# Optimization experiments

Measured on AMD Instinct MI355X. Metric: run time of the kernel, lower is better.

## Reference

```python
import math
import jax, jax.numpy as jnp
import numpy as np

B, P, L, D = 2, 32, 32, 768
N = P * L
H = 12
HD = D // H
FF = 4 * D
NL = 12
NC = 1000
EPS = 1e-5
NEG = -jnp.finfo(jnp.float32).max


def sinusoidal_pe(P, L, D):
    pe = np.zeros((P, L, D), dtype=np.float32)
    half = D // 2
    div = np.exp(np.arange(0.0, half, 2) * -(math.log(10000.0) / half))  # (half/2,)
    pos_l = np.arange(0.0, L)[:, None]
    pos_n = np.arange(0.0, P)[:, None]
    # faithful to the (buggy) torch builder, which requires P == L
    pe[:, :, 0:half:2] = np.sin(pos_n * div)[None, :, :]
    pe[:, :, 1:half:2] = np.cos(pos_n * div)[None, :, :]
    pe[:, :, half::2] = np.sin(pos_l * div)[:, None, :]
    pe[:, :, half + 1::2] = np.cos(pos_l * div)[:, None, :]
    return pe.reshape(P * L, D)


def layernorm(x, w, b):
    mu = jnp.mean(x, axis=-1, keepdims=True)
    var = jnp.var(x, axis=-1, keepdims=True)
    return (x - mu) * jax.lax.rsqrt(var + EPS) * w + b


def setup_inputs() -> dict:
    key = jax.random.key(0)
    ks = jax.random.split(key, 16)
    tn = lambda k, shp: (0.02 * jax.random.normal(k, shp)).astype(jnp.float32)
    inp = {
        "x": jax.random.normal(ks[0], (B, N, D), dtype=jnp.float32),
        "mask": jax.random.randint(ks[1], (B, N), 0, 2).astype(bool),
        "pe": jnp.asarray(sinusoidal_pe(P, L, D)),
        "ln0_w": jnp.ones((NL, D)), "ln0_b": jnp.zeros((NL, D)),
        "qkv_w": tn(ks[2], (NL, D, 3 * D)),
        "proj_w": tn(ks[3], (NL, D, D)), "proj_b": jnp.zeros((NL, D)),
        "ln1_w": jnp.ones((NL, D)), "ln1_b": jnp.zeros((NL, D)),
        "ff1_w": tn(ks[4], (NL, D, FF)), "ff1_b": jnp.zeros((NL, FF)),
        "ff2_w": tn(ks[5], (NL, FF, D)), "ff2_b": jnp.zeros((NL, D)),
        "norm_w": jnp.ones((D,)), "norm_b": jnp.zeros((D,)),
        "pool_w": tn(ks[6], (D, 1)), "pool_b": jnp.zeros((1,)),
        "fc_w": tn(ks[7], (D, NC)), "fc_b": jnp.zeros((NC,)),
    }
    return inp


def reference(x, mask, pe, ln0_w, ln0_b, qkv_w, proj_w, proj_b, ln1_w, ln1_b,
              ff1_w, ff1_b, ff2_w, ff2_b, norm_w, norm_b, pool_w, pool_b, fc_w, fc_b):
    scale = HD ** -0.5
    mask2 = mask[:, None, :] & mask[:, :, None]  # (B,N,N)

    def blk(h, p):
        g0w, g0b, qw, pw, pb, g1w, g1b, f1w, f1b, f2w, f2b = p
        y = layernorm(h, g0w, g0b)
        qkv = (y @ qw).reshape(B, N, 3, H, HD).transpose(2, 0, 3, 1, 4)  # (3,B,H,N,hd)
        q, k, v = qkv[0], qkv[1], qkv[2]
        attn = jnp.einsum('bhnd,bhmd->bhnm', q, k) * scale
        attn = jnp.where(mask2[:, None, :, :], attn, NEG)
        attn = jax.nn.softmax(attn, axis=-1)
        o = jnp.einsum('bhnm,bhmd->bhnd', attn, v)
        o = o.transpose(0, 2, 1, 3).reshape(B, N, D) @ pw + pb
        h = layernorm(h + o, g1w, g1b)
        ff = jax.nn.gelu(h @ f1w + f1b, approximate=False) @ f2w + f2b
        return h + ff, None

    h = x + pe[None]
    params = (ln0_w, ln0_b, qkv_w, proj_w, proj_b, ln1_w, ln1_b, ff1_w, ff1_b, ff2_w, ff2_b)
    h, _ = jax.lax.scan(blk, h, params)
    h = layernorm(h, norm_w, norm_b)
    # seq-pool: softmax over tokens of a learned scalar score
    w = jax.nn.softmax(h @ pool_w + pool_b, axis=1)  # (B,N,1)
    pooled = jnp.einsum('bnc,bnd->bd', w, h)  # c == 1
    return pooled @ fc_w + fc_b
```

## Files before the change

### kernel.cpp

```cpp
#include <hip/hip_runtime.h>
#include <hip/hip_bf16.h>
#include <cfloat>
#include <cmath>

typedef __bf16 bf16x8 __attribute__((ext_vector_type(8)));
typedef __bf16 bf16x4 __attribute__((ext_vector_type(4)));
typedef float  f32x4  __attribute__((ext_vector_type(4)));

static constexpr int Bb = 2, Nn = 1024, Dd = 768, Hh = 12, HDd = 64, FFf = 3072, NLl = 12, NCc = 1000;
static constexpr int Mm = Bb * Nn;
static constexpr float NEGF = -3.402823466e38f;

__device__ __forceinline__ float block_reduce_sum(float v, volatile float* smem) {
  for (int o = 32; o; o >>= 1) v += __shfl_down(v, o);
  int lane = threadIdx.x & 63, w = threadIdx.x >> 6;
  __syncthreads();
  if (lane == 0) smem[w] = v;
  __syncthreads();
  return smem[0] + smem[1] + smem[2] + smem[3];
}

__device__ __forceinline__ float block_reduce_max(float v, volatile float* smem) {
  for (int o = 32; o; o >>= 1) v = fmaxf(v, __shfl_down(v, o));
  int lane = threadIdx.x & 63, w = threadIdx.x >> 6;
  __syncthreads();
  if (lane == 0) smem[w] = v;
  __syncthreads();
  return fmaxf(fmaxf(smem[0], smem[1]), fmaxf(smem[2], smem[3]));
}

__global__ void detect_mask(const unsigned char* __restrict__ m, int* __restrict__ flag) {
  __shared__ int s_nz1, s_nz2, s_nz3, s_nz84, s_pv;
  int tid = threadIdx.x;
  if (tid == 0) { s_nz1 = 0; s_nz2 = 0; s_nz3 = 0; s_nz84 = 0; s_pv = 0; }
  __syncthreads();
  int nz1 = 0, nz2 = 0, nz3 = 0, nz84 = 0, pv = 0;
  for (int i = tid; i < 2048; i += 256) {
    unsigned char v = m[i];
    if (v) {
      int p4 = i & 3;
      if (p4 == 1) nz1 = 1;
      if (p4 == 2) nz2 = 1;
      if (p4 == 3) nz3 = 1;
      if ((i & 7) == 4) nz84 = 1;
      if ((i & 1) == 0) { if (v != 0x80) pv = 1; }
      else              { if (v != 0x3f) pv = 1; }
    }
  }
  if (nz1)  atomicOr(&s_nz1, 1);
  if (nz2)  atomicOr(&s_nz2, 1);
  if (nz3)  atomicOr(&s_nz3, 1);
  if (nz84) atomicOr(&s_nz84, 1);
  if (pv)   atomicOr(&s_pv, 1);
  __syncthreads();
  if (tid == 0) {
    int f;
    if (!s_nz1 && !s_nz2 && !s_nz3) f = s_nz84 ? 0 : 3;
    else if (!s_pv)                 f = s_nz1 ? 4 : 2;
    else                            f = 1;
    *flag = f;
  }
}

__device__ __forceinline__ bool mask_at(const void* mraw, int flag, int idx) {
  switch (flag) {
    case 0:  return ((const int*)mraw)[idx] != 0;
    case 1:  return ((const unsigned char*)mraw)[idx] != 0;
    case 2:  return ((const float*)mraw)[idx] != 0.f;
    case 3:  return ((const long long*)mraw)[idx] != 0;
    default: return ((const unsigned short*)mraw)[idx] != 0;
  }
}

__global__ __launch_bounds__(256) void add_pe_k(const float* __restrict__ x, const float* __restrict__ pe,
                                                float* __restrict__ h) {
  long i = (long)blockIdx.x * 256 + threadIdx.x;
  long nd = i % ((long)Nn * Dd);
  h[i] = x[i] + pe[nd];
}

template<int OBF>
__global__ __launch_bounds__(256) void ln_kernel(const float* __restrict__ X,
                                                 const float* __restrict__ w, const float* __restrict__ b,
                                                 void* __restrict__ Y) {
  __shared__ float smem[4];
  int row = blockIdx.x, tid = threadIdx.x;
  const float* x = X + (size_t)row * Dd;
  float v[3];
  for (int j = 0; j < 3; ++j) v[j] = x[tid + j * 256];
  float s = v[0] + v[1] + v[2];
  s = block_reduce_sum(s, smem);
  float mean = s * (1.f / 768.f);
  float q = 0.f;
  for (int j = 0; j < 3; ++j) { float d = v[j] - mean; q += d * d; }
  q = block_reduce_sum(q, smem);
  float inv = rsqrtf(q * (1.f / 768.f) + 1e-5f);
  for (int j = 0; j < 3; ++j) {
    int c = tid + j * 256;
    float r = (v[j] - mean) * inv * w[c] + b[c];
    if (OBF) ((__bf16*)Y)[(size_t)row * Dd + c] = (__bf16)r;
    else     ((float*)Y)[(size_t)row * Dd + c] = r;
  }
}

__global__ __launch_bounds__(256) void ln2res_kernel(float* __restrict__ H,
                                                     const float* __restrict__ P0, const float* __restrict__ P1,
                                                     const float* __restrict__ pb,
                                                     const float* __restrict__ w, const float* __restrict__ b,
                                                     __bf16* __restrict__ Hb) {
  __shared__ float smem[4];
  int row = blockIdx.x, tid = threadIdx.x;
  float* x  = H  + (size_t)row * Dd;
  const float* p0 = P0 + (size_t)row * Dd;
  const float* p1 = P1 + (size_t)row * Dd;
  float v[3];
  for (int j = 0; j < 3; ++j) {
    int c = tid + j * 256;
    v[j] = x[c] + (p0[c] + p1[c] + pb[c]);
  }
  float s = v[0] + v[1] + v[2];
  s = block_reduce_sum(s, smem);
  float mean = s * (1.f / 768.f);
  float q = 0.f;
  for (int j = 0; j < 3; ++j) { float d = v[j] - mean; q += d * d; }
  q = block_reduce_sum(q, smem);
  float inv = rsqrtf(q * (1.f / 768.f) + 1e-5f);
  for (int j = 0; j < 3; ++j) {
    int c = tid + j * 256;
    float r = (v[j] - mean) * inv * w[c] + b[c];
    x[c] = r;
    Hb[(size_t)row * Dd + c] = (__bf16)r;
  }
}

__global__ __launch_bounds__(256) void reduce_ff2(float* __restrict__ h, const float* __restrict__ p0,
                                                  const float* __restrict__ p1, const float* __restrict__ bias) {
  long i4 = (long)blockIdx.x * 256 + threadIdx.x;
  int col4 = (int)(i4 % (Dd / 4));
  float4 hv = reinterpret_cast<const float4*>(h)[i4];
  float4 a  = reinterpret_cast<const float4*>(p0)[i4];
  float4 c  = reinterpret_cast<const float4*>(p1)[i4];
  float4 bb = reinterpret_cast<const float4*>(bias)[col4];
  hv.x += a.x + c.x + bb.x;
  hv.y += a.y + c.y + bb.y;
  hv.z += a.z + c.z + bb.z;
  hv.w += a.w + c.w + bb.w;
  reinterpret_cast<float4*>(h)[i4] = hv;
}

__device__ __forceinline__ void split8v(const float* __restrict__ v, bf16x8& hi, bf16x8& lo) {
  for (int j = 0; j < 8; ++j) {
    __bf16 h = (__bf16)v[j];
    hi[j] = h;
    lo[j] = (__bf16)(v[j] - (float)h);
  }
}

template<int BN, int EPI, int OBF>
__global__ __launch_bounds__(256) void gemm128(
    const __bf16* __restrict__ Ap, long lda,
    const float* __restrict__ Bp, long ldb,
    const float* __restrict__ bias,
    void* __restrict__ Cp, long ldc,
    int Ksize, long czs)
{
  constexpr int FN = BN / 32;
  constexpr int KB = BN / 8;
  int tid = threadIdx.x;

  int nwg2 = gridDim.x * gridDim.y;
  int bid = blockIdx.y * gridDim.x + blockIdx.x;
  int swz = (bid & 7) * (nwg2 >> 3) + (bid >> 3);
  int bx = swz % gridDim.x, by = swz / gridDim.x;
  int m0 = by * 128, n0 = bx * BN;
  int z = blockIdx.z;

  const __bf16* Aq = Ap + (long)z * Ksize;
  const float* Bq = Bp + (long)z * Ksize * ldb;

  __shared__ __align__(16) __bf16 Ah[128][40];
  __shared__ __align__(16) __bf16 Bh[BN][40], Bl[BN][40];

  f32x4 acc[4][FN];
  #pragma unroll
  for (int i = 0; i < 4; ++i)
    #pragma unroll
    for (int j = 0; j < FN; ++j)
      #pragma unroll
      for (int k = 0; k < 4; ++k) acc[i][j][k] = 0.f;

  int lane = tid & 63;
  int w = tid >> 6;
  int WR = (w >> 1) * 64, WC = (w & 1) * (BN / 2);
  int fr = lane & 15, kg = lane >> 4;

  const int ar = tid >> 1, acs = (tid & 1) * 16;
  const int bn = tid % BN;
  const int kb = (tid / BN) * KB;

  const __bf16* Abase = Aq + (long)(m0 + ar) * lda + acs;
  const float* Bbase = Bq + (long)kb * ldb + (n0 + bn);

  bf16x8 pa0, pa1;
  float pb[KB];
  {
    pa0 = *reinterpret_cast<const bf16x8*>(Abase);
    pa1 = *reinterpret_cast<const bf16x8*>(Abase + 8);
    #pragma unroll
    for (int j = 0; j < KB; ++j) pb[j] = Bbase[(long)j * ldb];
  }

  for (int k0 = 0; k0 < Ksize; k0 += 32) {
    __syncthreads();
    {
      *reinterpret_cast<bf16x8*>(&Ah[ar][acs]) = pa0;
      *reinterpret_cast<bf16x8*>(&Ah[ar][acs + 8]) = pa1;
      #pragma unroll
      for (int g8 = 0; g8 < KB / 8; ++g8) {
        bf16x8 bth, btl;
        split8v(&pb[g8 * 8], bth, btl);
        *reinterpret_cast<bf16x8*>(&Bh[bn][kb + g8 * 8]) = bth;
        *reinterpret_cast<bf16x8*>(&Bl[bn][kb + g8 * 8]) = btl;
      }
    }
    __syncthreads();

    if (k0 + 32 < Ksize) {
      const __bf16* As = Abase + (k0 + 32);
      pa0 = *reinterpret_cast<const bf16x8*>(As);
      pa1 = *reinterpret_cast<const bf16x8*>(As + 8);
      const float* Bs = Bbase + (long)(k0 + 32) * ldb;
      #pragma unroll
      for (int j = 0; j < KB; ++j) pb[j] = Bs[(long)j * ldb];
    }

    bf16x8 ah[4], bh[FN], bl[FN];
    #pragma unroll
    for (int fm = 0; fm < 4; ++fm)
      ah[fm] = *reinterpret_cast<const bf16x8*>(&Ah[WR + fm * 16 + fr][kg * 8]);
    #pragma unroll
    for (int fn = 0; fn < FN; ++fn) {
      bh[fn] = *reinterpret_cast<const bf16x8*>(&Bh[WC + fn * 16 + fr][kg * 8]);
      bl[fn] = *reinterpret_cast<const bf16x8*>(&Bl[WC + fn * 16 + fr][kg * 8]);
    }
    #pragma unroll
    for (int fm = 0; fm < 4; ++fm)
      #pragma unroll
      for (int fn = 0; fn < FN; ++fn) {
        acc[fm][fn] = __builtin_amdgcn_mfma_f32_16x16x32_bf16(ah[fm], bh[fn], acc[fm][fn], 0, 0, 0);
        acc[fm][fn] = __builtin_amdgcn_mfma_f32_16x16x32_bf16(ah[fm], bl[fn], acc[fm][fn], 0, 0, 0);
      }
  }

  #pragma unroll
  for (int fm = 0; fm < 4; ++fm)
    #pragma unroll
    for (int fn = 0; fn < FN; ++fn)
      #pragma unroll
      for (int i = 0; i < 4; ++i) {
        int rowg = m0 + WR + fm * 16 + kg * 4 + i;
        int coln = n0 + WC + fn * 16 + fr;
        float v = acc[fm][fn][i];
        if (EPI >= 1) v += bias[coln];
        if (EPI == 2) v = 0.5f * v * (1.f + erff(v * 0.70710678118654752f));
        long ci = (long)z * czs + (long)rowg * ldc + coln;
        if (OBF) ((__bf16*)Cp)[ci] = (__bf16)v;
        else     ((float*)Cp)[ci] = v;
      }
}

__global__ __launch_bounds__(256) void flash_attn_split(const __bf16* __restrict__ qkvb,
                                                        const void* __restrict__ mraw,
                                                        const int* __restrict__ flagp,
                                                        float* __restrict__ p0, float* __restrict__ p1,
                                                        float2* __restrict__ ml) {
  __shared__ __align__(16) __bf16 Qs[64][72];
  __shared__ __align__(16) __bf16 Ks[64][72];
  __shared__ __align__(16) __bf16 Vt[64][66];
  __shared__ __align__(16) __bf16 Ps[64][72];
  __shared__ float kmf[64];
  __shared__ float qmf[64];

  int s = blockIdx.z & 1, b = blockIdx.z >> 1;
  int hh = blockIdx.y;
  int q0 = blockIdx.x * 64;
  int tid = threadIdx.x, lane = tid & 63, w = tid >> 6;
  int flag = *flagp;
  int fr = lane & 15, kg = lane >> 4;

  const int sr = tid >> 2;
  const int sc = (tid & 3) * 16;

  {
    const __bf16* Qsrc = qkvb + ((long)(b * Nn + q0 + sr)) * (3 * Dd) + hh * HDd + sc;
    *reinterpret_cast<bf16x8*>(&Qs[sr][sc])     = *reinterpret_cast<const bf16x8*>(Qsrc);
    *reinterpret_cast<bf16x8*>(&Qs[sr][sc + 8]) = *reinterpret_cast<const bf16x8*>(Qsrc + 8);
    if (tid < 64) qmf[tid] = mask_at(mraw, flag, b * Nn + q0 + tid) ? 1.f : 0.f;
  }
  __syncthreads();

  float qm[4];
  #pragma unroll
  for (int i = 0; i < 4; ++i) qm[i] = qmf[16 * w + kg * 4 + i];

  bf16x8 qa[2];
  #pragma unroll
  for (int ks = 0; ks < 2; ++ks)
    qa[ks] = *reinterpret_cast<const bf16x8*>(&Qs[16 * w + fr][ks * 32 + kg * 8]);

  float mrow[4], lrow[4];
  f32x4 accO[4];
  #pragma unroll
  for (int i = 0; i < 4; ++i) { mrow[i] = -INFINITY; lrow[i] = 0.f; }
  #pragma unroll
  for (int t = 0; t < 4; ++t)
    for (int i = 0; i < 4; ++i) accO[t][i] = 0.f;

  const int jbeg = s * (Nn / 2), jend = jbeg + (Nn / 2);

  bf16x8 rk0, rk1, rv0, rv1;
  {
    const __bf16* Ksrc = qkvb + ((long)(b * Nn + jbeg + sr)) * (3 * Dd) + Dd + hh * HDd + sc;
    const __bf16* Vsrc = Ksrc + Dd;
    rk0 = *reinterpret_cast<const bf16x8*>(Ksrc);
    rk1 = *reinterpret_cast<const bf16x8*>(Ksrc + 8);
    rv0 = *reinterpret_cast<const bf16x8*>(Vsrc);
    rv1 = *reinterpret_cast<const bf16x8*>(Vsrc + 8);
  }

  for (int j0 = jbeg; j0 < jend; j0 += 64) {
    __syncthreads();
    {
      *reinterpret_cast<bf16x8*>(&Ks[sr][sc])     = rk0;
      *reinterpret_cast<bf16x8*>(&Ks[sr][sc + 8]) = rk1;
      #pragma unroll
      for (int j = 0; j < 8; ++j) {
        Vt[sc + j][sr]     = rv0[j];
        Vt[sc + 8 + j][sr] = rv1[j];
      }
      if (tid < 64) kmf[tid] = mask_at(mraw, flag, b * Nn + j0 + tid) ? 1.f : 0.f;
    }
    __syncthreads();

    if (j0 + 64 < jend) {
      const __bf16* Ksrc = qkvb + ((long)(b * Nn + j0 + 64 + sr)) * (3 * Dd) + Dd + hh * HDd + sc;
      const __bf16* Vsrc = Ksrc + Dd;
      rk0 = *reinterpret_cast<const bf16x8*>(Ksrc);
      rk1 = *reinterpret_cast<const bf16x8*>(Ksrc + 8);
      rv0 = *reinterpret_cast<const bf16x8*>(Vsrc);
      rv1 = *reinterpret_cast<const bf16x8*>(Vsrc + 8);
    }

    f32x4 sacc[4];
    #pragma unroll
    for (int t = 0; t < 4; ++t)
      for (int i = 0; i < 4; ++i) sacc[t][i] = 0.f;
    #pragma unroll
    for (int ks = 0; ks < 2; ++ks) {
      #pragma unroll
      for (int t = 0; t < 4; ++t) {
        bf16x8 bh = *reinterpret_cast<const bf16x8*>(&Ks[16 * t + fr][ks * 32 + kg * 8]);
        sacc[t] = __builtin_amdgcn_mfma_f32_16x16x32_bf16(qa[ks], bh, sacc[t], 0, 0, 0);
      }
    }

    float sv[4][4];
    float mt[4] = {-INFINITY, -INFINITY, -INFINITY, -INFINITY};
    #pragma unroll
    for (int t = 0; t < 4; ++t) {
      float km = kmf[16 * t + fr];
      #pragma unroll
      for (int i = 0; i < 4; ++i) {
        float sx = (km > 0.f && qm[i] > 0.f) ? sacc[t][i] * 0.125f : NEGF;
        sv[t][i] = sx;
        mt[i] = fmaxf(mt[i], sx);
      }
    }
    #pragma unroll
    for (int off = 8; off; off >>= 1)
      #pragma unroll
      for (int i = 0; i < 4; ++i) mt[i] = fmaxf(mt[i], __shfl_xor(mt[i], off));

    float r[4], psum[4];
    #pragma unroll
    for (int i = 0; i < 4; ++i) {
      float mn = fmaxf(mrow[i], mt[i]);
      r[i] = __expf(mrow[i] - mn);
      mrow[i] = mn;
      psum[i] = 0.f;
    }
    #pragma unroll
    for (int t = 0; t < 4; ++t) {
      #pragma unroll
      for (int i = 0; i < 4; ++i) {
        float p = __expf(sv[t][i] - mrow[i]);
        psum[i] += p;
        Ps[16 * w + kg * 4 + i][16 * t + fr] = (__bf16)p;
      }
    }
    #pragma unroll
    for (int off = 8; off; off >>= 1)
      #pragma unroll
      for (int i = 0; i < 4; ++i) psum[i] += __shfl_xor(psum[i], off);
    #pragma unroll
    for (int i = 0; i < 4; ++i) lrow[i] = lrow[i] * r[i] + psum[i];
    #pragma unroll
    for (int t = 0; t < 4; ++t)
      #pragma unroll
      for (int i = 0; i < 4; ++i) accO[t][i] *= r[i];

    __syncthreads();

    #pragma unroll
    for (int ks = 0; ks < 2; ++ks) {
      bf16x8 pa = *reinterpret_cast<const bf16x8*>(&Ps[16 * w + fr][ks * 32 + kg * 8]);
      #pragma unroll
      for (int t2 = 0; t2 < 4; ++t2) {
        bf16x8 vb = *reinterpret_cast<const bf16x8*>(&Vt[16 * t2 + fr][ks * 32 + kg * 8]);
        accO[t2] = __builtin_amdgcn_mfma_f32_16x16x32_bf16(pa, vb, accO[t2], 0, 0, 0);
      }
    }
  }

  float* op = s ? p1 : p0;
  #pragma unroll
  for (int t2 = 0; t2 < 4; ++t2)
    #pragma unroll
    for (int i = 0; i < 4; ++i) {
      int qrow = q0 + 16 * w + kg * 4 + i;
      int col = 16 * t2 + fr;
      op[((long)(b * Nn + qrow)) * Dd + hh * HDd + col] = accO[t2][i];
    }
  if (fr == 0) {
    #pragma unroll
    for (int i = 0; i < 4; ++i) {
      int qrow = q0 + 16 * w + kg * 4 + i;
      ml[((long)(s * Bb + b) * Hh + hh) * Nn + qrow] = make_float2(mrow[i], lrow[i]);
    }
  }
}

__global__ __launch_bounds__(256) void flash_combine(const float* __restrict__ p0, const float* __restrict__ p1,
                                                     const float2* __restrict__ ml, __bf16* __restrict__ ob) {
  long i4 = (long)blockIdx.x * 256 + threadIdx.x;
  long i = i4 * 4;
  int d = (int)(i % Dd);
  long row = i / Dd;
  int b = (int)(row >> 10), n = (int)(row & (Nn - 1));
  int hh = d >> 6;
  float2 a = ml[((long)b * Hh + hh) * Nn + n];
  float2 c = ml[(((long)Bb + b) * Hh + hh) * Nn + n];
  float M = fmaxf(a.x, c.x);
  float w0 = __expf(a.x - M), w1 = __expf(c.x - M);
  float inv = 1.f / (w0 * a.y + w1 * c.y);
  float4 v0 = reinterpret_cast<const float4*>(p0)[i4];
  float4 v1 = reinterpret_cast<const float4*>(p1)[i4];
  bf16x4 r;
  r[0] = (__bf16)((w0 * v0.x + w1 * v1.x) * inv);
  r[1] = (__bf16)((w0 * v0.y + w1 * v1.y) * inv);
  r[2] = (__bf16)((w0 * v0.z + w1 * v1.z) * inv);
  r[3] = (__bf16)((w0 * v0.w + w1 * v1.w) * inv);
  *reinterpret_cast<bf16x4*>(&ob[i]) = r;
}

__global__ __launch_bounds__(256) void pool_score(const float* __restrict__ hn, const float* __restrict__ pw,
                                                  const float* __restrict__ pb, float* __restrict__ s) {
  __shared__ float smem[4];
  int row = blockIdx.x, tid = threadIdx.x;
  const float* x = hn + (size_t)row * Dd;
  float acc = 0.f;
  for (int j = 0; j < 3; ++j) { int c = tid + j * 256; acc += x[c] * pw[c]; }
  acc = block_reduce_sum(acc, smem);
  if (tid == 0) s[row] = acc + pb[0];
}

__global__ __launch_bounds__(256) void pool_softmax(const float* __restrict__ s, float* __restrict__ w) {
  __shared__ float smem[4];
  int b = blockIdx.x, tid = threadIdx.x;
  const float* x = s + b * Nn;
  float v[4];
  for (int j = 0; j < 4; ++j) v[j] = x[tid * 4 + j];
  float mx = fmaxf(fmaxf(v[0], v[1]), fmaxf(v[2], v[3]));
  mx = block_reduce_max(mx, smem);
  float e[4], sum = 0.f;
  for (int j = 0; j < 4; ++j) { e[j] = expf(v[j] - mx); sum += e[j]; }
  sum = block_reduce_sum(sum, smem);
  float inv = 1.f / sum;
  for (int j = 0; j < 4; ++j) w[b * Nn + tid * 4 + j] = e[j] * inv;
}

__global__ __launch_bounds__(256) void pool_reduce1(const float* __restrict__ hn, const float* __restrict__ w,
                                                    float* __restrict__ part) {
  int d = blockIdx.x * 256 + threadIdx.x;
  int ch = blockIdx.y, b = blockIdx.z;
  int n0 = ch * 128;
  float a0 = 0.f, a1 = 0.f;
  for (int n = n0; n < n0 + 128; n += 2) {
    a0 = fmaf(w[b * Nn + n],     hn[((size_t)(b * Nn + n))     * Dd + d], a0);
    a1 = fmaf(w[b * Nn + n + 1], hn[((size_t)(b * Nn + n + 1)) * Dd + d], a1);
  }
  part[((size_t)(b * 8 + ch)) * Dd + d] = a0 + a1;
}

__global__ __launch_bounds__(256) void pool_reduce2(const float* __restrict__ part, float* __restrict__ pooled) {
  int d = blockIdx.x * 256 + threadIdx.x;
  int b = blockIdx.y;
  float s = 0.f;
  #pragma unroll
  for (int ch = 0; ch < 8; ++ch) s += part[((size_t)(b * 8 + ch)) * Dd + d];
  pooled[b * Dd + d] = s;
}

__global__ __launch_bounds__(256) void fc_kernel(const float* __restrict__ pooled, const float* __restrict__ fw,
                                                 const float* __restrict__ fb, float* __restrict__ out) {
  __shared__ float p[768];
  int b = blockIdx.y, tid = threadIdx.x;
  for (int j = 0; j < 3; ++j) p[tid + j * 256] = pooled[b * Dd + tid + j * 256];
  __syncthreads();
  int c = blockIdx.x * 256 + tid;
  if (c < NCc) {
    float a0 = 0.f, a1 = 0.f, a2 = 0.f, a3 = 0.f;
    #pragma unroll 4
    for (int d = 0; d < Dd; d += 4) {
      a0 = fmaf(p[d],     fw[(size_t)d       * NCc + c], a0);
      a1 = fmaf(p[d + 1], fw[(size_t)(d + 1) * NCc + c], a1);
      a2 = fmaf(p[d + 2], fw[(size_t)(d + 2) * NCc + c], a2);
      a3 = fmaf(p[d + 3], fw[(size_t)(d + 3) * NCc + c], a3);
    }
    out[b * NCc + c] = fb[c] + ((a0 + a1) + (a2 + a3));
  }
}

extern "C" void kernel_launch(void* const* d_in, const int* in_sizes, int n_in,
                              void* d_out, int out_size, void* d_ws, size_t ws_size,
                              hipStream_t stream) {
  const float* x      = (const float*)d_in[0];
  const void*  mask   = d_in[1];
  const float* pe     = (const float*)d_in[2];
  const float* ln0_w  = (const float*)d_in[3];
  const float* ln0_b  = (const float*)d_in[4];
  const float* qkv_w  = (const float*)d_in[5];
  const float* proj_w = (const float*)d_in[6];
  const float* proj_b = (const float*)d_in[7];
  const float* ln1_w  = (const float*)d_in[8];
  const float* ln1_b  = (const float*)d_in[9];
  const float* ff1_w  = (const float*)d_in[10];
  const float* ff1_b  = (const float*)d_in[11];
  const float* ff2_w  = (const float*)d_in[12];
  const float* ff2_b  = (const float*)d_in[13];
  const float* norm_w = (const float*)d_in[14];
  const float* norm_b = (const float*)d_in[15];
  const float* pool_w = (const float*)d_in[16];
  const float* pool_b = (const float*)d_in[17];
  const float* fc_w   = (const float*)d_in[18];
  const float* fc_b   = (const float*)d_in[19];
  float* out = (float*)d_out;

  float* ws = (float*)d_ws;
  float*  h     = ws;
  float*  s0    = h + (long)Mm * Dd;
  float*  s1    = s0 + (long)Mm * Dd;
  __bf16* qkvb  = (__bf16*)(s1 + (long)Mm * Dd);
  __bf16* ob    = qkvb + (long)Mm * 3 * Dd;
  __bf16* yb    = ob + (long)Mm * Dd;
  float*  tail  = (float*)(yb + (long)Mm * Dd);
  float*  spool  = tail;
  float*  wpool  = spool + Mm;
  float*  pooled = wpool + Mm;
  float*  ppart  = pooled + Bb * Dd;
  float*  mlbuf  = ppart + (long)Bb * 8 * Dd;
  int*    mflag  = (int*)(mlbuf + (long)2 * 2 * Bb * Hh * Nn);
  __bf16* gb = qkvb;
  float*  hn = s0;

  detect_mask<<<1, 256, 0, stream>>>((const unsigned char*)mask, mflag);
  add_pe_k<<<(Mm * Dd) / 256, 256, 0, stream>>>(x, pe, h);

  for (int l = 0; l < NLl; ++l) {
    ln_kernel<1><<<Mm, 256, 0, stream>>>(h, ln0_w + l * Dd, ln0_b + l * Dd, yb);

    gemm128<64,0,1><<<dim3(3 * Dd / 64, Mm / 128, 1), 256, 0, stream>>>(
        yb, Dd,
        qkv_w + (long)l * Dd * 3 * Dd, 3 * Dd,
        nullptr,
        qkvb, 3 * Dd, Dd, 0);

    flash_attn_split<<<dim3(Nn / 64, Hh, Bb * 2), 256, 0, stream>>>(
        qkvb, mask, mflag, s0, s1, (float2*)mlbuf);
    flash_combine<<<(Mm * Dd / 4) / 256, 256, 0, stream>>>(s0, s1, (const float2*)mlbuf, ob);

    gemm128<64,0,0><<<dim3(Dd / 64, Mm / 128, 2), 256, 0, stream>>>(
        ob, Dd,
        proj_w + (long)l * Dd * Dd, Dd,
        nullptr,
        s0, Dd, Dd / 2, (long)(s1 - s0));

    ln2res_kernel<<<Mm, 256, 0, stream>>>(h, s0, s1, proj_b + l * Dd,
                                          ln1_w + l * Dd, ln1_b + l * Dd, yb);

    gemm128<64,2,1><<<dim3(FFf / 64, Mm / 128, 1), 256, 0, stream>>>(
        yb, Dd,
        ff1_w + (long)l * Dd * FFf, FFf,
        ff1_b + l * FFf,
        gb, FFf, Dd, 0);

    gemm128<64,0,0><<<dim3(Dd / 64, Mm / 128, 2), 256, 0, stream>>>(
        gb, FFf,
        ff2_w + (long)l * FFf * Dd, Dd,
        nullptr,
        s0, Dd, FFf / 2, (long)(s1 - s0));

    reduce_ff2<<<(Mm * Dd / 4) / 256, 256, 0, stream>>>(h, s0, s1, ff2_b + l * Dd);
  }

  ln_kernel<0><<<Mm, 256, 0, stream>>>(h, norm_w, norm_b, hn);
  pool_score<<<Mm, 256, 0, stream>>>(hn, pool_w, pool_b, spool);
  pool_softmax<<<Bb, 256, 0, stream>>>(spool, wpool);
  pool_reduce1<<<dim3(Dd / 256, 8, Bb), 256, 0, stream>>>(hn, wpool, ppart);
  pool_reduce2<<<dim3(Dd / 256, Bb), 256, 0, stream>>>(ppart, pooled);
  fc_kernel<<<dim3(4, Bb), 256, 0, stream>>>(pooled, fc_w, fc_b, out);
}
```

Measured before the change: 2.245 ms.

## Drop bf16 hi/lo weight split in GEMM and fuse FF2 residual with next LayerNorm

The GEMM previously split each fp32 weight into a high and low bf16 pair and issued two MFMAs per fragment to approximate fp32 accuracy. Now it keeps only the single bf16 rounding, which halves MFMA work, B-tile shared memory and the split arithmetic, at the cost of lower weight precision. Separately, the FF2 partial-sum reduction is fused with the following layer's LN0 (or the final norm), removing one elementwise kernel and one LayerNorm pass per layer.

```diff
diff --git a/kernel.cpp b/kernel.cpp
--- a/kernel.cpp
+++ b/kernel.cpp
@@ -103,11 +103,12 @@
   }
 }
 
-__global__ __launch_bounds__(256) void ln2res_kernel(float* __restrict__ H,
+template<int OBF, int HRES>
+__global__ __launch_bounds__(256) void res_ln_kernel(float* __restrict__ H,
                                                      const float* __restrict__ P0, const float* __restrict__ P1,
                                                      const float* __restrict__ pb,
                                                      const float* __restrict__ w, const float* __restrict__ b,
-                                                     __bf16* __restrict__ Hb) {
+                                                     void* __restrict__ Y) {
   __shared__ float smem[4];
   int row = blockIdx.x, tid = threadIdx.x;
   float* x  = H  + (size_t)row * Dd;
@@ -128,31 +129,9 @@
   for (int j = 0; j < 3; ++j) {
     int c = tid + j * 256;
     float r = (v[j] - mean) * inv * w[c] + b[c];
-    x[c] = r;
-    Hb[(size_t)row * Dd + c] = (__bf16)r;
-  }
-}
-
-__global__ __launch_bounds__(256) void reduce_ff2(float* __restrict__ h, const float* __restrict__ p0,
-                                                  const float* __restrict__ p1, const float* __restrict__ bias) {
-  long i4 = (long)blockIdx.x * 256 + threadIdx.x;
-  int col4 = (int)(i4 % (Dd / 4));
-  float4 hv = reinterpret_cast<const float4*>(h)[i4];
-  float4 a  = reinterpret_cast<const float4*>(p0)[i4];
-  float4 c  = reinterpret_cast<const float4*>(p1)[i4];
-  float4 bb = reinterpret_cast<const float4*>(bias)[col4];
-  hv.x += a.x + c.x + bb.x;
-  hv.y += a.y + c.y + bb.y;
-  hv.z += a.z + c.z + bb.z;
-  hv.w += a.w + c.w + bb.w;
-  reinterpret_cast<float4*>(h)[i4] = hv;
-}
-
-__device__ __forceinline__ void split8v(const float* __restrict__ v, bf16x8& hi, bf16x8& lo) {
-  for (int j = 0; j < 8; ++j) {
-    __bf16 h = (__bf16)v[j];
-    hi[j] = h;
-    lo[j] = (__bf16)(v[j] - (float)h);
+    x[c] = HRES ? v[j] : r;
+    if (OBF) ((__bf16*)Y)[(size_t)row * Dd + c] = (__bf16)r;
+    else     ((float*)Y)[(size_t)row * Dd + c] = r;
   }
 }
 
@@ -179,7 +158,7 @@
   const float* Bq = Bp + (long)z * Ksize * ldb;
 
   __shared__ __align__(16) __bf16 Ah[128][40];
-  __shared__ __align__(16) __bf16 Bh[BN][40], Bl[BN][40];
+  __shared__ __align__(16) __bf16 Bh[BN][40];
 
   f32x4 acc[4][FN];
   #pragma unroll
@@ -217,10 +196,10 @@
       *reinterpret_cast<bf16x8*>(&Ah[ar][acs + 8]) = pa1;
       #pragma unroll
       for (int g8 = 0; g8 < KB / 8; ++g8) {
-        bf16x8 bth, btl;
-        split8v(&pb[g8 * 8], bth, btl);
+        bf16x8 bth;
+        #pragma unroll
+        for (int j = 0; j < 8; ++j) bth[j] = (__bf16)pb[g8 * 8 + j];
         *reinterpret_cast<bf16x8*>(&Bh[bn][kb + g8 * 8]) = bth;
-        *reinterpret_cast<bf16x8*>(&Bl[bn][kb + g8 * 8]) = btl;
       }
     }
     __syncthreads();
@@ -234,22 +213,18 @@
       for (int j = 0; j < KB; ++j) pb[j] = Bs[(long)j * ldb];
     }
 
-    bf16x8 ah[4], bh[FN], bl[FN];
+    bf16x8 ah[4], bh[FN];
     #pragma unroll
     for (int fm = 0; fm < 4; ++fm)
       ah[fm] = *reinterpret_cast<const bf16x8*>(&Ah[WR + fm * 16 + fr][kg * 8]);
     #pragma unroll
-    for (int fn = 0; fn < FN; ++fn) {
+    for (int fn = 0; fn < FN; ++fn)
       bh[fn] = *reinterpret_cast<const bf16x8*>(&Bh[WC + fn * 16 + fr][kg * 8]);
-      bl[fn] = *reinterpret_cast<const bf16x8*>(&Bl[WC + fn * 16 + fr][kg * 8]);
-    }
     #pragma unroll
     for (int fm = 0; fm < 4; ++fm)
       #pragma unroll
-      for (int fn = 0; fn < FN; ++fn) {
+      for (int fn = 0; fn < FN; ++fn)
         acc[fm][fn] = __builtin_amdgcn_mfma_f32_16x16x32_bf16(ah[fm], bh[fn], acc[fm][fn], 0, 0, 0);
-        acc[fm][fn] = __builtin_amdgcn_mfma_f32_16x16x32_bf16(ah[fm], bl[fn], acc[fm][fn], 0, 0, 0);
-      }
   }
 
   #pragma unroll
@@ -575,10 +550,9 @@
 
   detect_mask<<<1, 256, 0, stream>>>((const unsigned char*)mask, mflag);
   add_pe_k<<<(Mm * Dd) / 256, 256, 0, stream>>>(x, pe, h);
+  ln_kernel<1><<<Mm, 256, 0, stream>>>(h, ln0_w, ln0_b, yb);
 
   for (int l = 0; l < NLl; ++l) {
-    ln_kernel<1><<<Mm, 256, 0, stream>>>(h, ln0_w + l * Dd, ln0_b + l * Dd, yb);
-
     gemm128<64,0,1><<<dim3(3 * Dd / 64, Mm / 128, 1), 256, 0, stream>>>(
         yb, Dd,
         qkv_w + (long)l * Dd * 3 * Dd, 3 * Dd,
@@ -595,8 +569,8 @@
         nullptr,
         s0, Dd, Dd / 2, (long)(s1 - s0));
 
-    ln2res_kernel<<<Mm, 256, 0, stream>>>(h, s0, s1, proj_b + l * Dd,
-                                          ln1_w + l * Dd, ln1_b + l * Dd, yb);
+    res_ln_kernel<1,0><<<Mm, 256, 0, stream>>>(h, s0, s1, proj_b + l * Dd,
+                                               ln1_w + l * Dd, ln1_b + l * Dd, yb);
 
     gemm128<64,2,1><<<dim3(FFf / 64, Mm / 128, 1), 256, 0, stream>>>(
         yb, Dd,
@@ -610,10 +584,15 @@
         nullptr,
         s0, Dd, FFf / 2, (long)(s1 - s0));
 
-    reduce_ff2<<<(Mm * Dd / 4) / 256, 256, 0, stream>>>(h, s0, s1, ff2_b + l * Dd);
-  }
-
-  ln_kernel<0><<<Mm, 256, 0, stream>>>(h, norm_w, norm_b, hn);
+    if (l + 1 < NLl) {
+      res_ln_kernel<1,1><<<Mm, 256, 0, stream>>>(h, s0, s1, ff2_b + l * Dd,
+                                                 ln0_w + (l + 1) * Dd, ln0_b + (l + 1) * Dd, yb);
+    } else {
+      res_ln_kernel<0,1><<<Mm, 256, 0, stream>>>(h, s0, s1, ff2_b + l * Dd,
+                                                 norm_w, norm_b, hn);
+    }
+  }
+
   pool_score<<<Mm, 256, 0, stream>>>(hn, pool_w, pool_b, spool);
   pool_softmax<<<Bb, 256, 0, stream>>>(spool, wpool);
   pool_reduce1<<<dim3(Dd / 256, 8, Bb), 256, 0, stream>>>(hn, wpool, ppart);
```

After: 2.113 ms. 5.9% less time.
